# Optimization experiments

Hardware: AMD Instinct MI355X
Metric: run time of the kernel (lower is better)

## Reference

```python
import jax, jax.numpy as jnp
import numpy as np
import math

HIDDEN = 4096
N_HEADS = 32
HEAD_DIM = HIDDEN // N_HEADS
MAX_POS = 4096
BASE = 10000.0
NEG_INF = jnp.finfo(jnp.float32).min


def rotate_half(x):
    x1, x2 = jnp.split(x, 2, axis=-1)
    return jnp.concatenate((-x2, x1), axis=-1)


def rope_tables(seq_len, dtype=jnp.float32):
    inv_freq = 1.0 / (BASE ** (jnp.arange(0, HEAD_DIM, 2, dtype=jnp.float32) / HEAD_DIM))
    t = jnp.arange(seq_len, dtype=jnp.float32)
    freqs = jnp.einsum('i,j->ij', t, inv_freq)  # [S, D/2]
    emb = jnp.concatenate((freqs, freqs), axis=-1)  # [S, D]
    return jnp.cos(emb).astype(dtype), jnp.sin(emb).astype(dtype)


def setup_inputs() -> dict:
    key = jax.random.key(0)
    k1, k2, k3 = jax.random.split(key, 3)
    bsz, q_len = 2, 2048
    hidden_states = jax.random.normal(k1, (bsz, q_len, HIDDEN), dtype=jnp.float32)
    # causal additive mask [bsz, 1, q, q]: 0 on/below diag, large-negative above
    causal = jnp.triu(jnp.full((q_len, q_len), NEG_INF, dtype=jnp.float32), k=1)
    attention_mask = jnp.broadcast_to(causal[None, None], (bsz, 1, q_len, q_len))
    position_ids = jnp.broadcast_to(jnp.arange(q_len, dtype=jnp.int64)[None], (bsz, q_len))
    W_pack = jax.random.normal(k2, (3 * HIDDEN, HIDDEN), dtype=jnp.float32) * (1.0 / math.sqrt(HIDDEN))
    W_o = jax.random.normal(k3, (HIDDEN, HIDDEN), dtype=jnp.float32) * (1.0 / math.sqrt(HIDDEN))
    return {"hidden_states": hidden_states, "attention_mask": attention_mask,
            "position_ids": position_ids, "W_pack": W_pack, "W_o": W_o}


def reference(hidden_states, attention_mask, position_ids, W_pack, W_o):
    bsz, q_len, _ = hidden_states.shape
    proj = jnp.einsum('bsh,oh->bso', hidden_states, W_pack)  # [B,S,3H]
    q, k, v = jnp.split(proj, 3, axis=-1)
    def shape(x):
        return x.reshape(bsz, q_len, N_HEADS, HEAD_DIM).transpose(0, 2, 1, 3)  # [B,nH,S,D]
    q, k, v = shape(q), shape(k), shape(v)
    cos, sin = rope_tables(q_len, hidden_states.dtype)
    cos = cos[position_ids][:, None]  # [B,1,S,D]
    sin = sin[position_ids][:, None]
    q = q * cos + rotate_half(q) * sin
    k = k * cos + rotate_half(k) * sin
    scores = jnp.einsum('bhqd,bhkd->bhqk', q, k) / math.sqrt(HEAD_DIM)
    scores = scores + attention_mask
    scores = jnp.maximum(scores, NEG_INF)
    w = jax.nn.softmax(scores.astype(jnp.float32), axis=-1).astype(q.dtype)
    out = jnp.einsum('bhqk,bhkd->bhqd', w, v)
    out = out.transpose(0, 2, 1, 3).reshape(bsz, q_len, HIDDEN)
    return jnp.einsum('bsh,oh->bso', out, W_o)
```

## Files before the change

### kernel.cpp

```cpp
#include <hip/hip_runtime.h>
#include <hip/hip_bf16.h>

typedef __bf16 bf16x8 __attribute__((ext_vector_type(8)));
typedef float f32x4 __attribute__((ext_vector_type(4)));

#define HIDDEN 4096
#define NH 32
#define HD 128
#define SEQ 2048
#define BATCH 2
#define MTOT 4096
#define QKV 12288

__device__ __forceinline__ void async16(const void* g, void* l) {
    __builtin_amdgcn_global_load_lds(
        (const __attribute__((address_space(1))) void*)(uintptr_t)g,
        (__attribute__((address_space(3))) void*)(uint32_t)(uintptr_t)l,
        16, 0, 0);
}

__device__ __forceinline__ uint4 ld8(const __hip_bfloat16* p) { return *(const uint4*)p; }
__device__ __forceinline__ uint4 ld8(const float* p) {
    float4 a = *(const float4*)p;
    float4 b = *(const float4*)(p + 4);
    __hip_bfloat16 t[8];
    t[0] = __float2bfloat16(a.x); t[1] = __float2bfloat16(a.y);
    t[2] = __float2bfloat16(a.z); t[3] = __float2bfloat16(a.w);
    t[4] = __float2bfloat16(b.x); t[5] = __float2bfloat16(b.y);
    t[6] = __float2bfloat16(b.z); t[7] = __float2bfloat16(b.w);
    return *(uint4*)t;
}

__device__ __forceinline__ void stc(__hip_bfloat16* C, size_t i, float v) { C[i] = __float2bfloat16(v); }
__device__ __forceinline__ void stc(float* C, size_t i, float v) { C[i] = v; }

__global__ __launch_bounds__(256) void cvt_bf16(const float* __restrict__ src,
                                                __hip_bfloat16* __restrict__ dst, int n8) {
    int i = blockIdx.x * 256 + threadIdx.x;
    if (i < n8) *(uint4*)&dst[(size_t)i * 8] = ld8(&src[(size_t)i * 8]);
}

template <typename TC>
__global__ __launch_bounds__(512) void gemm_256(const __hip_bfloat16* __restrict__ A,
                                                const __hip_bfloat16* __restrict__ Bt,
                                                TC* __restrict__ C,
                                                int M, int N, int K, int lda) {
    __shared__ __align__(16) __hip_bfloat16 As[2][256][64];
    __shared__ __align__(16) __hip_bfloat16 Bs[2][256][64];
    const int bn = blockIdx.x * 256, bm = blockIdx.y * 256;
    const int tid = threadIdx.x, wave = tid >> 6, lane = tid & 63;
    const int wm = wave >> 2, wn = wave & 3;
    const int row16 = lane & 15, quad = lane >> 4;
    const int srow = lane >> 3;
    const int schunk = (lane & 7) ^ srow;
    const __hip_bfloat16* Ab = A + (size_t)(bm + wave * 8 + srow) * lda + schunk * 8;
    const __hip_bfloat16* Bb = Bt + (size_t)(bn + wave * 8 + srow) * K + schunk * 8;
    const int NT = K >> 6;

    f32x4 acc[8][4] = {};

    auto stage = [&](int t) {
        const int s = t & 1;
        const size_t kt = (size_t)t << 6;
#pragma unroll
        for (int k = 0; k < 4; ++k) {
            async16(Ab + (size_t)(k * 64) * lda + kt, &As[s][k * 64 + wave * 8][0]);
            async16(Bb + (size_t)(k * 64) * K  + kt, &Bs[s][k * 64 + wave * 8][0]);
        }
    };

    stage(0);

    for (int t = 0; t < NT; ++t) {
        const int s = t & 1;
        asm volatile("s_waitcnt vmcnt(0)" ::: "memory");
        __builtin_amdgcn_s_barrier();
        if (t + 1 < NT) stage(t + 1);
        __builtin_amdgcn_sched_barrier(0);
        const int pcb = (quad ^ (row16 & 7)) * 8;
        const int pcb1 = ((4 + quad) ^ (row16 & 7)) * 8;
#pragma unroll
        for (int ks = 0; ks < 2; ++ks) {
            const int pc = ks ? pcb1 : pcb;
            bf16x8 af[8], bf[4];
#pragma unroll
            for (int i = 0; i < 8; ++i)
                af[i] = *(const bf16x8*)&As[s][wm * 128 + i * 16 + row16][pc];
#pragma unroll
            for (int j = 0; j < 4; ++j)
                bf[j] = *(const bf16x8*)&Bs[s][wn * 64 + j * 16 + row16][pc];
            __builtin_amdgcn_s_setprio(1);
#pragma unroll
            for (int i = 0; i < 8; ++i)
#pragma unroll
                for (int j = 0; j < 4; ++j)
                    acc[i][j] = __builtin_amdgcn_mfma_f32_16x16x32_bf16(af[i], bf[j], acc[i][j], 0, 0, 0);
            __builtin_amdgcn_s_setprio(0);
        }
    }

    const int col0 = bn + wn * 64 + row16;
    const int row0 = bm + wm * 128 + quad * 4;
#pragma unroll
    for (int i = 0; i < 8; ++i)
#pragma unroll
        for (int j = 0; j < 4; ++j)
#pragma unroll
            for (int rg = 0; rg < 4; ++rg)
                stc(C, (size_t)(row0 + i * 16 + rg) * N + col0 + j * 16, acc[i][j][rg]);
}

template <typename TA, typename TB, typename TC>
__global__ __launch_bounds__(256) void gemm_bt(const TA* __restrict__ A,
                                               const TB* __restrict__ Bt,
                                               TC* __restrict__ C,
                                               int M, int N, int K, int lda) {
    __shared__ __align__(16) __hip_bfloat16 As[128][32];
    __shared__ __align__(16) __hip_bfloat16 Bs[128][32];
    const int bn = blockIdx.x * 128, bm = blockIdx.y * 128;
    const int tid = threadIdx.x, wave = tid >> 6, lane = tid & 63;
    const int wm = (wave >> 1) * 64, wn = (wave & 1) * 64;
    const int row16 = lane & 15, quad = lane >> 4;
    const int arow = tid >> 2;
    const int acol = (tid & 3) * 8;

    f32x4 acc[4][4] = {};

    for (int kt = 0; kt < K; kt += 32) {
        __syncthreads();
#pragma unroll
        for (int it = 0; it < 2; ++it) {
            int r = arow + it * 64;
            *(uint4*)&As[r][acol] = ld8(&A[(size_t)(bm + r) * lda + kt + acol]);
            *(uint4*)&Bs[r][acol] = ld8(&Bt[(size_t)(bn + r) * K + kt + acol]);
        }
        __syncthreads();
        bf16x8 af[4], bf[4];
#pragma unroll
        for (int i = 0; i < 4; ++i) af[i] = *(const bf16x8*)&As[wm + i * 16 + row16][quad * 8];
#pragma unroll
        for (int j = 0; j < 4; ++j) bf[j] = *(const bf16x8*)&Bs[wn + j * 16 + row16][quad * 8];
#pragma unroll
        for (int i = 0; i < 4; ++i)
#pragma unroll
            for (int j = 0; j < 4; ++j)
                acc[i][j] = __builtin_amdgcn_mfma_f32_16x16x32_bf16(af[i], bf[j], acc[i][j], 0, 0, 0);
    }
    const int col0 = bn + wn + row16;
    const int row0 = bm + wm + quad * 4;
#pragma unroll
    for (int i = 0; i < 4; ++i)
#pragma unroll
        for (int j = 0; j < 4; ++j)
#pragma unroll
            for (int rg = 0; rg < 4; ++rg)
                stc(C, (size_t)(row0 + i * 16 + rg) * N + col0 + j * 16, acc[i][j][rg]);
}

__global__ __launch_bounds__(256) void rope_kernel(__hip_bfloat16* __restrict__ proj) {
    int t = blockIdx.x * 256 + threadIdx.x;
    int j = t & 63;
    int head = (t >> 6) & 31;
    int mat = (t >> 11) & 1;
    int row = t >> 12;
    int pos = row & (SEQ - 1);
    float invf = __expf(-(float)j * 0.14391156514261f);
    float ang = (float)pos * invf;
    float rev = ang * 0.15915494309189535f;
    rev -= floorf(rev);
    float arad = rev * 6.283185307179586f;
    float sn = __sinf(arad);
    float cs = __cosf(arad);
    if (mat == 0) {
        sn *= 0.08838834764831845f;
        cs *= 0.08838834764831845f;
    }
    size_t base = (size_t)row * QKV + mat * HIDDEN + head * HD + j;
    float x1 = __bfloat162float(proj[base]);
    float x2 = __bfloat162float(proj[base + 64]);
    proj[base]      = __float2bfloat16(x1 * cs - x2 * sn);
    proj[base + 64] = __float2bfloat16(x2 * cs + x1 * sn);
}

__global__ __launch_bounds__(256) void transpose_v(const __hip_bfloat16* __restrict__ proj,
                                                   __hip_bfloat16* __restrict__ vtg) {
    __shared__ __hip_bfloat16 Ls[64][132];
    const int st = blockIdx.x, bh = blockIdx.y;
    const int b = bh >> 5, h = bh & 31;
    const int s0 = st << 6;
    const int tid = threadIdx.x;
    const __hip_bfloat16* vb = proj + (size_t)b * SEQ * QKV + 2 * HIDDEN + h * HD;
    for (int i = tid; i < 1024; i += 256) {
        int r = i >> 4, c = (i & 15) << 3;
        uint4 raw = *(const uint4*)&vb[(size_t)(s0 + r) * QKV + c];
        *(uint2*)&Ls[r][c]     = make_uint2(raw.x, raw.y);
        *(uint2*)&Ls[r][c + 4] = make_uint2(raw.z, raw.w);
    }
    __syncthreads();
    __hip_bfloat16* ob = vtg + (size_t)bh * HD * SEQ + s0;
    for (int t = tid; t < 1024; t += 256) {
        int d = t >> 3, sc = (t & 7) << 3;
        __hip_bfloat16 tmp[8];
#pragma unroll
        for (int x = 0; x < 8; ++x) tmp[x] = Ls[sc + x][d];
        *(uint4*)&ob[(size_t)d * SEQ + sc] = *(uint4*)tmp;
    }
}

__global__ __launch_bounds__(512) void attn_mfma(__hip_bfloat16* __restrict__ proj,
                                                 const __hip_bfloat16* __restrict__ vtg) {
    __shared__ __align__(16) __hip_bfloat16 Kf[2][16][512];
    __shared__ __align__(16) __hip_bfloat16 Vf[2][16][512];
    __shared__ __align__(16) __hip_bfloat16 Ps[8][32][72];
    const int nwg = gridDim.x * gridDim.y;
    const int f  = blockIdx.y * gridDim.x + blockIdx.x;
    const int f2 = (f & 7) * (nwg >> 3) + (f >> 3);
    const int qt = f2 & 7;
    const int bh = f2 >> 3;
    const int b = bh >> 5, h = bh & 31;
    const int q0 = qt << 8;
    const int tid = threadIdx.x, wave = tid >> 6, lane = tid & 63;
    const int row16 = lane & 15, quad = lane >> 4;

    __hip_bfloat16* qb = proj + (size_t)b * SEQ * QKV + h * HD;
    const __hip_bfloat16* kb = qb + HIDDEN;
    const __hip_bfloat16* vp = vtg + (size_t)bh * HD * SEQ;

    const int wbase = q0 + wave * 32;

    const int b0 = 2 * wave, b1 = 2 * wave + 1;
    const __hip_bfloat16* ks0 = kb + (size_t)((b0 >> 2) * 16 + row16) * QKV + (b0 & 3) * 32 + quad * 8;
    const __hip_bfloat16* ks1 = kb + (size_t)((b1 >> 2) * 16 + row16) * QKV + (b1 & 3) * 32 + quad * 8;
    const __hip_bfloat16* vs0 = vp + (size_t)((b0 >> 1) * 16 + row16) * SEQ + (b0 & 1) * 32 + quad * 8;
    const __hip_bfloat16* vs1 = vp + (size_t)((b1 >> 1) * 16 + row16) * SEQ + (b1 & 1) * 32 + quad * 8;

    auto stage = [&](int kt) {
        const int s = kt & 1;
        const int k0 = kt << 6;
        async16(ks0 + (size_t)k0 * QKV, &Kf[s][b0][0]);
        async16(ks1 + (size_t)k0 * QKV, &Kf[s][b1][0]);
        async16(vs0 + k0,               &Vf[s][b0][0]);
        async16(vs1 + k0,               &Vf[s][b1][0]);
    };

    bf16x8 qf[2][4];
#pragma unroll
    for (int qr = 0; qr < 2; ++qr) {
        const __hip_bfloat16* qrow = qb + (size_t)(wbase + qr * 16 + row16) * QKV + quad * 8;
#pragma unroll
        for (int s = 0; s < 4; ++s) qf[qr][s] = *(const bf16x8*)(qrow + s * 32);
    }

    f32x4 oa[2][8] = {};
    float m_i[2][4], l_i[2][4];
#pragma unroll
    for (int qr = 0; qr < 2; ++qr)
#pragma unroll
        for (int r = 0; r < 4; ++r) { m_i[qr][r] = -3.0e38f; l_i[qr][r] = 0.f; }

    stage(0);
    asm volatile("s_waitcnt vmcnt(0)" ::: "memory");
    __builtin_amdgcn_s_barrier();
    __builtin_amdgcn_sched_barrier(0);

    const int ktmax = 4 * qt + 3;
    for (int kt = 0; kt <= ktmax; ++kt) {
        const int s = kt & 1;
        const int k0 = kt << 6;
        if (kt < ktmax) stage(kt + 1);
        if (k0 <= wbase + 31) {
            f32x4 sf[2][4] = {};
#pragma unroll
            for (int nt = 0; nt < 4; ++nt) {
                bf16x8 kf[4];
#pragma unroll
                for (int ks = 0; ks < 4; ++ks)
                    kf[ks] = *(const bf16x8*)&Kf[s][nt * 4 + ks][lane * 8];
#pragma unroll
                for (int qr = 0; qr < 2; ++qr)
#pragma unroll
                    for (int ks = 0; ks < 4; ++ks)
                        sf[qr][nt] = __builtin_amdgcn_mfma_f32_16x16x32_bf16(qf[qr][ks], kf[ks], sf[qr][nt], 0, 0, 0);
            }
            if (k0 + 63 > wbase) {
#pragma unroll
                for (int qr = 0; qr < 2; ++qr)
#pragma unroll
                    for (int nt = 0; nt < 4; ++nt) {
                        int key = k0 + nt * 16 + row16;
#pragma unroll
                        for (int rg = 0; rg < 4; ++rg)
                            if (key > wbase + qr * 16 + quad * 4 + rg) sf[qr][nt][rg] = -3.0e38f;
                    }
            }
#pragma unroll
            for (int qr = 0; qr < 2; ++qr) {
                float alpha[4], rs[4];
#pragma unroll
                for (int rg = 0; rg < 4; ++rg) {
                    float mx = fmaxf(fmaxf(sf[qr][0][rg], sf[qr][1][rg]), fmaxf(sf[qr][2][rg], sf[qr][3][rg]));
#pragma unroll
                    for (int off = 8; off > 0; off >>= 1) mx = fmaxf(mx, __shfl_xor(mx, off));
                    float mn = fmaxf(m_i[qr][rg], mx);
                    alpha[rg] = __expf(m_i[qr][rg] - mn);
                    m_i[qr][rg] = mn;
                    rs[rg] = 0.f;
                }
#pragma unroll
                for (int nt = 0; nt < 4; ++nt)
#pragma unroll
                    for (int rg = 0; rg < 4; ++rg) {
                        float p = __expf(sf[qr][nt][rg] - m_i[qr][rg]);
                        rs[rg] += p;
                        Ps[wave][qr * 16 + quad * 4 + rg][nt * 16 + row16] = __float2bfloat16(p);
                    }
#pragma unroll
                for (int rg = 0; rg < 4; ++rg) {
#pragma unroll
                    for (int off = 8; off > 0; off >>= 1) rs[rg] += __shfl_xor(rs[rg], off);
                    l_i[qr][rg] = l_i[qr][rg] * alpha[rg] + rs[rg];
                }
#pragma unroll
                for (int dt = 0; dt < 8; ++dt)
#pragma unroll
                    for (int rg = 0; rg < 4; ++rg) oa[qr][dt][rg] *= alpha[rg];
            }
            __builtin_amdgcn_wave_barrier();
            bf16x8 pf[2][2];
#pragma unroll
            for (int qr = 0; qr < 2; ++qr) {
                pf[qr][0] = *(const bf16x8*)&Ps[wave][qr * 16 + row16][quad * 8];
                pf[qr][1] = *(const bf16x8*)&Ps[wave][qr * 16 + row16][32 + quad * 8];
            }
#pragma unroll
            for (int dt = 0; dt < 8; ++dt) {
                bf16x8 v0 = *(const bf16x8*)&Vf[s][dt * 2][lane * 8];
                bf16x8 v1 = *(const bf16x8*)&Vf[s][dt * 2 + 1][lane * 8];
#pragma unroll
                for (int qr = 0; qr < 2; ++qr) {
                    oa[qr][dt] = __builtin_amdgcn_mfma_f32_16x16x32_bf16(pf[qr][0], v0, oa[qr][dt], 0, 0, 0);
                    oa[qr][dt] = __builtin_amdgcn_mfma_f32_16x16x32_bf16(pf[qr][1], v1, oa[qr][dt], 0, 0, 0);
                }
            }
        }
        asm volatile("s_waitcnt vmcnt(0)" ::: "memory");
        __builtin_amdgcn_s_barrier();
        __builtin_amdgcn_sched_barrier(0);
    }
#pragma unroll
    for (int qr = 0; qr < 2; ++qr)
#pragma unroll
        for (int rg = 0; rg < 4; ++rg) {
            float inv = 1.0f / l_i[qr][rg];
            __hip_bfloat16* orow = qb + (size_t)(wbase + qr * 16 + quad * 4 + rg) * QKV;
#pragma unroll
            for (int dt = 0; dt < 8; ++dt)
                orow[dt * 16 + row16] = __float2bfloat16(oa[qr][dt][rg] * inv);
        }
}

extern "C" void kernel_launch(void* const* d_in, const int* in_sizes, int n_in,
                              void* d_out, int out_size, void* d_ws, size_t ws_size,
                              hipStream_t stream) {
    const float* hs = (const float*)d_in[0];
    const float* Wp = (const float*)d_in[3];
    const float* Wo = (const float*)d_in[4];
    float* out = (float*)d_out;

    const size_t SZ_PROJ = (size_t)MTOT * QKV;
    const size_t SZ_H    = (size_t)MTOT * HIDDEN;
    const size_t SZ_WP   = (size_t)QKV * HIDDEN;
    const size_t need = (SZ_PROJ + SZ_H + SZ_WP + SZ_H) * sizeof(__hip_bfloat16);

    __hip_bfloat16* proj = (__hip_bfloat16*)d_ws;

    if (ws_size >= need) {
        __hip_bfloat16* hsb = proj + SZ_PROJ;
        __hip_bfloat16* Wpb = hsb + SZ_H;
        __hip_bfloat16* Wob = Wpb + SZ_WP;
        __hip_bfloat16* vtg = hsb;

        cvt_bf16<<<dim3(SZ_H / 8 / 256), dim3(256), 0, stream>>>(hs, hsb, SZ_H / 8);
        cvt_bf16<<<dim3(SZ_WP / 8 / 256), dim3(256), 0, stream>>>(Wp, Wpb, SZ_WP / 8);
        cvt_bf16<<<dim3(SZ_H / 8 / 256), dim3(256), 0, stream>>>(Wo, Wob, SZ_H / 8);
        gemm_256<<<dim3(QKV / 256, MTOT / 256), dim3(512), 0, stream>>>(hsb, Wpb, proj, MTOT, QKV, HIDDEN, HIDDEN);
        rope_kernel<<<dim3((MTOT * 2 * NH * 64) / 256), dim3(256), 0, stream>>>(proj);
        transpose_v<<<dim3(SEQ / 64, BATCH * NH), dim3(256), 0, stream>>>(proj, vtg);
        attn_mfma<<<dim3(SEQ / 256, BATCH * NH), dim3(512), 0, stream>>>(proj, vtg);
        gemm_256<<<dim3(HIDDEN / 256, MTOT / 256), dim3(512), 0, stream>>>(proj, Wob, out, MTOT, HIDDEN, HIDDEN, QKV);
    } else {
        __hip_bfloat16* vtg = proj + SZ_PROJ;
        gemm_bt<<<dim3(QKV / 128, MTOT / 128), dim3(256), 0, stream>>>(hs, Wp, proj, MTOT, QKV, HIDDEN, HIDDEN);
        rope_kernel<<<dim3((MTOT * 2 * NH * 64) / 256), dim3(256), 0, stream>>>(proj);
        transpose_v<<<dim3(SEQ / 64, BATCH * NH), dim3(256), 0, stream>>>(proj, vtg);
        attn_mfma<<<dim3(SEQ / 256, BATCH * NH), dim3(512), 0, stream>>>(proj, vtg);
        gemm_bt<<<dim3(HIDDEN / 128, MTOT / 128), dim3(256), 0, stream>>>(proj, Wo, out, MTOT, HIDDEN, HIDDEN, QKV);
    }
}
```

Before: 1.110 ms.

## Split GEMM k-tile into four phases interleaving LDS reads, prefetch and MFMA

Restructures the 256x256 GEMM main loop into four phases per k-tile, each loading a half set of A fragments (and B fragments on even phases) and then running 16 MFMAs. The next tile's async global-to-LDS loads are spread across the first two phases instead of being issued all at once, and block barriers are added around each phase to keep waves in lockstep, ping-pong style. The aim is better overlap of LDS reads and global prefetch with MFMA work and lower register pressure from fewer live A fragments, at the cost of many extra barriers per tile.

```diff
diff --git a/kernel.cpp b/kernel.cpp
--- a/kernel.cpp
+++ b/kernel.cpp
@@ -59,43 +59,57 @@
 
     f32x4 acc[8][4] = {};
 
-    auto stage = [&](int t) {
-        const int s = t & 1;
-        const size_t kt = (size_t)t << 6;
+    {
 #pragma unroll
         for (int k = 0; k < 4; ++k) {
-            async16(Ab + (size_t)(k * 64) * lda + kt, &As[s][k * 64 + wave * 8][0]);
-            async16(Bb + (size_t)(k * 64) * K  + kt, &Bs[s][k * 64 + wave * 8][0]);
+            async16(Ab + (size_t)(k * 64) * lda, &As[0][k * 64 + wave * 8][0]);
+            async16(Bb + (size_t)(k * 64) * K,  &Bs[0][k * 64 + wave * 8][0]);
         }
-    };
-
-    stage(0);
+    }
 
     for (int t = 0; t < NT; ++t) {
-        const int s = t & 1;
+        const int s = t & 1, s1 = s ^ 1;
+        const size_t kt1 = (size_t)(t + 1) << 6;
+        const bool more = (t + 1 < NT);
         asm volatile("s_waitcnt vmcnt(0)" ::: "memory");
         __builtin_amdgcn_s_barrier();
-        if (t + 1 < NT) stage(t + 1);
         __builtin_amdgcn_sched_barrier(0);
-        const int pcb = (quad ^ (row16 & 7)) * 8;
-        const int pcb1 = ((4 + quad) ^ (row16 & 7)) * 8;
-#pragma unroll
-        for (int ks = 0; ks < 2; ++ks) {
-            const int pc = ks ? pcb1 : pcb;
-            bf16x8 af[8], bf[4];
-#pragma unroll
-            for (int i = 0; i < 8; ++i)
-                af[i] = *(const bf16x8*)&As[s][wm * 128 + i * 16 + row16][pc];
-#pragma unroll
-            for (int j = 0; j < 4; ++j)
-                bf[j] = *(const bf16x8*)&Bs[s][wn * 64 + j * 16 + row16][pc];
+        bf16x8 bf[4];
+#pragma unroll
+        for (int p = 0; p < 4; ++p) {
+            const int ks = p >> 1, ih = p & 1;
+            const int pc = ((ks * 4 + quad) ^ (row16 & 7)) * 8;
+            bf16x8 af[4];
+            if (ih == 0) {
+#pragma unroll
+                for (int j = 0; j < 4; ++j)
+                    bf[j] = *(const bf16x8*)&Bs[s][wn * 64 + j * 16 + row16][pc];
+            }
+#pragma unroll
+            for (int i = 0; i < 4; ++i)
+                af[i] = *(const bf16x8*)&As[s][wm * 128 + (ih * 4 + i) * 16 + row16][pc];
+            if (more && p == 0) {
+#pragma unroll
+                for (int k = 0; k < 4; ++k)
+                    async16(Ab + (size_t)(k * 64) * lda + kt1, &As[s1][k * 64 + wave * 8][0]);
+            }
+            if (more && p == 1) {
+#pragma unroll
+                for (int k = 0; k < 4; ++k)
+                    async16(Bb + (size_t)(k * 64) * K + kt1, &Bs[s1][k * 64 + wave * 8][0]);
+            }
+            __builtin_amdgcn_sched_barrier(0);
+            __builtin_amdgcn_s_barrier();
+            asm volatile("s_waitcnt lgkmcnt(0)" ::: "memory");
+            __builtin_amdgcn_sched_barrier(0);
             __builtin_amdgcn_s_setprio(1);
 #pragma unroll
-            for (int i = 0; i < 8; ++i)
+            for (int i = 0; i < 4; ++i)
 #pragma unroll
                 for (int j = 0; j < 4; ++j)
-                    acc[i][j] = __builtin_amdgcn_mfma_f32_16x16x32_bf16(af[i], bf[j], acc[i][j], 0, 0, 0);
+                    acc[ih * 4 + i][j] = __builtin_amdgcn_mfma_f32_16x16x32_bf16(af[i], bf[j], acc[ih * 4 + i][j], 0, 0, 0);
             __builtin_amdgcn_s_setprio(0);
+            __builtin_amdgcn_s_barrier();
         }
     }
 
```

Result: no change. 1.105 ms (-0.5%).
